# Kernel optimization log

Hardware: AMD Instinct MI355X
Metric: run time of the kernel (lower is better)

Reference implementation:

```python
import jax, jax.numpy as jnp
import numpy as np
import math

DIM = 1024
D_IN = 2048      # expand * dim
N = 16           # d_state
NG = 32          # ngroups
DT_RANK = 64     # ceil(dim/16)
D_CONV = 4
B, L = 2, 1024


def setup_inputs() -> dict:
    key = jax.random.key(0)
    ks = jax.random.split(key, 10)
    nrm = lambda k, shp, s: jax.random.normal(k, shp, jnp.float32) * s
    x = jax.random.normal(ks[0], (B, L, DIM), jnp.float32)
    latent = jnp.zeros((B, NG, D_IN, N), jnp.float32)
    W_in = nrm(ks[1], (2 * D_IN, DIM), 0.02)          # in_proj (no bias)
    conv_w = nrm(ks[2], (D_IN, 1, D_CONV), 0.1)        # depthwise conv weight
    conv_b = nrm(ks[3], (D_IN,), 0.02)                 # conv bias
    W_x = nrm(ks[4], (DT_RANK + 2 * N, D_IN), 0.02)    # x_proj (no bias)
    W_dt = nrm(ks[5], (D_IN, DT_RANK), 0.02)           # dt_proj weight
    b_dt = nrm(ks[6], (D_IN,), 0.1)                    # dt_proj bias
    W_out = nrm(ks[7], (DIM, D_IN), 0.02)              # out_proj (no bias)
    A_log = jnp.log(jnp.tile(jnp.arange(1, N + 1, dtype=jnp.float32), (D_IN, 1)))
    D = jnp.ones((D_IN,), jnp.float32)
    W_cattn = nrm(ks[8], (3 * N, N), 0.02)             # c_attn (no bias)
    return dict(x=x, latent=latent, W_in=W_in, conv_w=conv_w, conv_b=conv_b,
                W_x=W_x, W_dt=W_dt, b_dt=b_dt, W_out=W_out, A_log=A_log,
                D=D, W_cattn=W_cattn)


def _scan_op(e1, e2):
    a1, b1 = e1
    a2, b2 = e2
    return a2 * a1, a2 * b1 + b2


def reference(x, latent, W_in, conv_w, conv_b, W_x, W_dt, b_dt, W_out, A_log, D, W_cattn):
    b, l, _ = x.shape
    xr = x @ W_in.T                                  # [b,l,2*d_in]
    u, res = xr[..., :D_IN], xr[..., D_IN:]
    # depthwise causal conv1d (padding d_conv-1 then truncate to l == left-pad)
    uc = jnp.transpose(u, (0, 2, 1))                 # [b,d_in,l]
    uc = jax.lax.conv_general_dilated(
        uc, conv_w, window_strides=(1,), padding=[(D_CONV - 1, 0)],
        feature_group_count=D_IN, dimension_numbers=('NCH', 'OIH', 'NCH'))
    uc = uc + conv_b[None, :, None]
    u = jax.nn.silu(jnp.transpose(uc, (0, 2, 1)))    # [b,l,d_in]

    A = -jnp.exp(A_log)                              # [d_in,n]
    x_dbl = u @ W_x.T                                # [b,l,dt_rank+2n]
    delta = jax.nn.softplus(x_dbl[..., :DT_RANK] @ W_dt.T + b_dt)  # [b,l,d_in]
    Bm = x_dbl[..., DT_RANK:DT_RANK + N]             # [b,l,n]
    Cm = x_dbl[..., DT_RANK + N:]                    # [b,l,n]

    dA = jnp.exp(delta[..., None] * A)               # [b,l,d_in,n]
    dBu = delta[..., None] * Bm[:, :, None, :] * u[..., None]  # [b,l,d_in,n]

    pg = l // NG
    dA = dA.reshape(b, NG, pg, D_IN, N)
    dBu = dBu.reshape(b, NG, pg, D_IN, N)
    Cg = Cm.reshape(b, NG, pg, N)
    dBu = dBu.at[:, :, 0].add(latent)                # inject group latent

    # parallel scan of h_t = dA_t * h_{t-1} + dBu_t within each group
    _, hs = jax.lax.associative_scan(_scan_op, (dA, dBu), axis=2)
    y = jnp.einsum('bgpdn,bgpn->bgpd', hs, Cg).reshape(b, l, D_IN)
    y = y + u * D

    # latent communication: causal attention over group latents (initial latent, per source)
    qkv = latent[:, :-1] @ W_cattn.T                 # [b,ng-1,d_in,3n]
    q, k, v = jnp.split(qkv, 3, axis=-1)
    G = NG - 1
    q = q.reshape(b, G, -1)
    k = k.reshape(b, G, -1)
    v = v.reshape(b, G, -1)
    scale = 1.0 / math.sqrt(D_IN * N)
    scores = (q @ jnp.swapaxes(k, 1, 2)) * scale     # [b,G,G]
    mask = jnp.tril(jnp.ones((G, G), bool))
    scores = jnp.where(mask, scores, -jnp.inf)
    attn = jax.nn.softmax(scores, axis=-1)
    lat = (attn @ v).reshape(b, G, D_IN, N)
    lat_out = jnp.concatenate([jnp.zeros((b, 1, D_IN, N), x.dtype), lat], axis=1)

    out = (y * jax.nn.silu(res)) @ W_out.T           # [b,l,dim]
    return out, lat_out
```

## Files before the change

### kernel.cpp

```cpp
#include <hip/hip_runtime.h>
#include <stdint.h>

typedef uint16_t u16;
typedef u16   u16x4  __attribute__((ext_vector_type(4)));
typedef u16   u16x8  __attribute__((ext_vector_type(8)));
typedef __bf16 bf16x8 __attribute__((ext_vector_type(8)));
typedef float f32x4  __attribute__((ext_vector_type(4)));

__device__ __forceinline__ float b2f(u16 x) {
    union { uint32_t u; float f; } c; c.u = ((uint32_t)x) << 16; return c.f;
}
__device__ __forceinline__ u16 f2b(float f) {
    union { float f; uint32_t u; } c; c.f = f;
    uint32_t r = c.u + 0x7FFFu + ((c.u >> 16) & 1u);
    return (u16)(r >> 16);
}
__device__ __forceinline__ float silu_f(float x) { return x / (1.f + __expf(-x)); }

__device__ __forceinline__ void gload16(const u16* g, u16* l) {
    __builtin_amdgcn_global_load_lds(
        (const __attribute__((address_space(1))) void*)(g),
        (__attribute__((address_space(3))) void*)(l), 16, 0, 0);
}

__device__ __forceinline__ int dtype_flag_block(const u16* __restrict__ xraw) {
    __shared__ int bad;
    if (threadIdx.x == 0) bad = 0;
    __syncthreads();
    float v = b2f(xraw[threadIdx.x]);
    if (!(fabsf(v) < 1000.f)) atomicAdd(&bad, 1);
    __syncthreads();
    return bad;
}

struct CvtArgs {
    const void* s[13];
    u16* d[13];
    int cum[14];
    int total;
};
__global__ __launch_bounds__(256) void cvt_all_k(CvtArgs a, const u16* __restrict__ xraw)
{
    int flag = dtype_flag_block(xraw);
    int u4 = blockIdx.x * 256 + threadIdx.x;
    if (u4 >= a.total) return;
    int seg = 0;
    while (u4 >= a.cum[seg + 1]) seg++;
    int local = u4 - a.cum[seg];
    const void* s = a.s[seg];
    u16x4 o;
    if (s == nullptr) {
        o[0] = o[1] = o[2] = o[3] = 0;
    } else if (flag) {
        f32x4 vv = ((const f32x4*)s)[local];
        for (int e = 0; e < 4; e++) o[e] = f2b(vv[e]);
    } else {
        o = ((const u16x4*)s)[local];
    }
    *(u16x4*)(a.d[seg] + (size_t)local * 4) = o;
}

template<int EPI, int TN>
__device__ __forceinline__ void gemm_core(
    int bx, int by, int bz,
    const u16* __restrict__ A, const u16* __restrict__ B,
    int Kc, int lda, int ldb,
    u16* __restrict__ Cb, float* __restrict__ Cf, int ldc, int ncols,
    const u16* __restrict__ bias, size_t zslab)
{
    constexpr int NJ = TN / 32;
    constexpr int BT = TN / 32;
    __shared__ __align__(16) u16 lA[128 * 64];
    __shared__ __align__(16) u16 lB[TN * 64];
    const int tid  = threadIdx.x;
    const int wave = tid >> 6, lane = tid & 63;
    const int quad = lane >> 4, l16 = lane & 15;
    const int wm = wave & 1, wn = wave >> 1;
    const int row0 = by * 128, col0 = bx * TN;
    const int kbeg = bz * Kc;

    f32x4 acc[4][NJ];
    const f32x4 zf = {0.f, 0.f, 0.f, 0.f};
    for (int i = 0; i < 4; i++) for (int j = 0; j < NJ; j++) acc[i][j] = zf;

    const u16* Ap[4]; const u16* Bp[BT];
    int lbaseA[4], lbaseB[BT];
    for (int t = 0; t < 4; t++) {
        int c = t * 256 + tid;
        int r = c >> 3, s = c & 7;
        int q = (s - (r >> 1)) & 7;
        Ap[t] = A + (size_t)(row0 + r) * lda + q * 8 + kbeg;
        lbaseA[t] = (t * 256 + wave * 64) * 8;
    }
    for (int t = 0; t < BT; t++) {
        int c = t * 256 + tid;
        int r = c >> 3, s = c & 7;
        int q = (s - (r >> 1)) & 7;
        Bp[t] = B + (size_t)(col0 + r) * ldb + q * 8 + kbeg;
        lbaseB[t] = (t * 256 + wave * 64) * 8;
    }

    for (int k0 = 0; k0 < Kc; k0 += 64) {
        for (int t = 0; t < 4; t++) gload16(Ap[t] + k0, &lA[lbaseA[t]]);
        for (int t = 0; t < BT; t++) gload16(Bp[t] + k0, &lB[lbaseB[t]]);
        __syncthreads();
        for (int half = 0; half < 2; half++) {
            bf16x8 af[4], bfr[NJ];
            for (int i = 0; i < 4; i++) {
                int r = wm * 64 + i * 16 + l16;
                int s = (half * 4 + quad + (r >> 1)) & 7;
                af[i] = *(const bf16x8*)&lA[r * 64 + s * 8];
            }
            for (int j = 0; j < NJ; j++) {
                int r = wn * (TN / 2) + j * 16 + l16;
                int s = (half * 4 + quad + (r >> 1)) & 7;
                bfr[j] = *(const bf16x8*)&lB[r * 64 + s * 8];
            }
            for (int i = 0; i < 4; i++)
                for (int j = 0; j < NJ; j++)
                    acc[i][j] = __builtin_amdgcn_mfma_f32_16x16x32_bf16(af[i], bfr[j], acc[i][j], 0, 0, 0);
        }
        __syncthreads();
    }

    float* dstf = (EPI == 2) ? (Cf + (size_t)bz * zslab) : Cf;
    for (int i = 0; i < 4; i++) {
        int mb = row0 + wm * 64 + i * 16 + quad * 4;
        for (int j = 0; j < NJ; j++) {
            int n = col0 + wn * (TN / 2) + j * 16 + l16;
            if (n >= ncols) continue;
            if (EPI == 0) {
                for (int v = 0; v < 4; v++)
                    Cb[(size_t)(mb + v) * ldc + n] = f2b(acc[i][j][v]);
            } else if (EPI == 1) {
                float bv = b2f(bias[n]);
                for (int v = 0; v < 4; v++) {
                    float xx = acc[i][j][v] + bv;
                    dstf[(size_t)(mb + v) * ldc + n] =
                        fmaxf(xx, 0.f) + __logf(1.f + __expf(-fabsf(xx)));
                }
            } else {
                for (int v = 0; v < 4; v++)
                    dstf[(size_t)(mb + v) * ldc + n] = acc[i][j][v];
            }
        }
    }
}

template<int EPI, int TN>
__global__ __launch_bounds__(256) void gemm_bt(
    const u16* __restrict__ A, const u16* __restrict__ B,
    int Kc, int lda, int ldb,
    u16* __restrict__ Cb, float* __restrict__ Cf, int ldc, int ncols,
    const u16* __restrict__ bias, size_t zslab)
{
    gemm_core<EPI, TN>(blockIdx.x, blockIdx.y, blockIdx.z,
                       A, B, Kc, lda, ldb, Cb, Cf, ldc, ncols, bias, zslab);
}

__global__ __launch_bounds__(256) void redc_k(
    const float* __restrict__ part, u16* __restrict__ dst)
{
    int gid = blockIdx.x * 256 + threadIdx.x;
    int idx = gid * 4;
    f32x4 s = {0.f, 0.f, 0.f, 0.f};
    for (int sl = 0; sl < 16; sl++) {
        f32x4 p = *(const f32x4*)&part[(size_t)sl * 262144 + idx];
        for (int e = 0; e < 4; e++) s[e] += p[e];
    }
    u16x4 o;
    for (int e = 0; e < 4; e++) o[e] = f2b(s[e]);
    *(u16x4*)&dst[idx] = o;
}

__global__ __launch_bounds__(256) void conv_silu_k(
    const u16* __restrict__ xr, const u16* __restrict__ cw,
    const u16* __restrict__ cb, u16* __restrict__ u)
{
    int tid = threadIdx.x;
    int bl  = blockIdx.x;
    int l   = bl & 1023;
    int d0  = tid * 8;
    float acc[8];
    u16x8 bias = *(const u16x8*)&cb[d0];
    for (int j = 0; j < 8; j++) acc[j] = b2f(bias[j]);
    union { u16x8 v[4]; u16 s[32]; } wb;
    for (int t = 0; t < 4; t++) wb.v[t] = *(const u16x8*)&cw[d0 * 4 + t * 8];
    for (int t = 0; t < 4; t++) {
        int ls = l - 3 + t;
        if (ls < 0) continue;
        u16x8 xv = *(const u16x8*)&xr[(size_t)(bl - 3 + t) * 4096 + d0];
        for (int j = 0; j < 8; j++) acc[j] += b2f(xv[j]) * b2f(wb.s[j * 4 + t]);
    }
    u16x8 o;
    for (int j = 0; j < 8; j++) o[j] = f2b(silu_f(acc[j]));
    *(u16x8*)&u[(size_t)bl * 2048 + d0] = o;
}

__global__ __launch_bounds__(256) void scan_qkv_k(
    const float* __restrict__ delta, const u16* __restrict__ u,
    const u16* __restrict__ xr, const u16* __restrict__ xdbl,
    const u16* __restrict__ latent, const u16* __restrict__ Alog,
    const u16* __restrict__ Dp, u16* __restrict__ yg,
    const u16* __restrict__ Wc, u16* __restrict__ q, u16* __restrict__ k,
    u16* __restrict__ v)
{
    __shared__ float sm[1024];
    int tid = threadIdx.x;
    int bid = blockIdx.x;
    if (bid < 512) {
        float (*Bs)[16] = (float(*)[16])sm;
        float (*Cs)[16] = (float(*)[16])(sm + 512);
        int dblk = bid & 7, bg = bid >> 3;
        int d = dblk * 256 + tid;
        for (int idx = tid; idx < 512; idx += 256) {
            int p = idx >> 4, n = idx & 15;
            const u16* xp = &xdbl[(size_t)(bg * 32 + p) * 128];
            Bs[p][n] = b2f(xp[64 + n]);
            Cs[p][n] = b2f(xp[80 + n]);
        }
        __syncthreads();
        float a[16], h[16];
        {
            u16x8 a0 = *(const u16x8*)&Alog[(size_t)d * 16];
            u16x8 a1 = *(const u16x8*)&Alog[(size_t)d * 16 + 8];
            u16x8 l0 = *(const u16x8*)&latent[((size_t)bg * 2048 + d) * 16];
            u16x8 l1 = *(const u16x8*)&latent[((size_t)bg * 2048 + d) * 16 + 8];
            for (int n = 0; n < 8; n++) {
                a[n] = -__expf(b2f(a0[n])); a[8 + n] = -__expf(b2f(a1[n]));
                h[n] = b2f(l0[n]);          h[8 + n] = b2f(l1[n]);
            }
        }
        float Dd = b2f(Dp[d]);
        for (int p = 0; p < 32; p++) {
            size_t row = (size_t)bg * 32 + p;
            float dlt = delta[row * 2048 + d];
            float uu  = b2f(u[row * 2048 + d]);
            float db  = dlt * uu;
            float y = 0.f;
            if (p == 0) {
                for (int n = 0; n < 16; n++) { h[n] += db * Bs[0][n]; y += h[n] * Cs[0][n]; }
            } else {
                for (int n = 0; n < 16; n++) {
                    float w = __expf(dlt * a[n]);
                    h[n] = w * h[n] + db * Bs[p][n];
                    y += h[n] * Cs[p][n];
                }
            }
            float rs = b2f(xr[row * 4096 + 2048 + d]);
            yg[row * 2048 + d] = f2b((y + uu * Dd) * silu_f(rs));
        }
    } else {
        float (*Ws)[16] = (float(*)[16])sm;
        for (int i = tid; i < 768; i += 256) Ws[i >> 4][i & 15] = b2f(Wc[i]);
        __syncthreads();
        int gid = (bid - 512) * 256 + tid;
        int d = gid & 2047;
        int bi = gid >> 11;
        int b = bi / 31, i = bi - b * 31;
        const u16* lp = &latent[(((size_t)b * 32 + i) * 2048 + d) * 16];
        float lv[16];
        {
            u16x8 l0 = *(const u16x8*)lp, l1 = *(const u16x8*)(lp + 8);
            for (int m = 0; m < 8; m++) { lv[m] = b2f(l0[m]); lv[8 + m] = b2f(l1[m]); }
        }
        u16* outs[3] = {q, k, v};
        for (int pl = 0; pl < 3; pl++) {
            u16x8 o0, o1;
            for (int n = 0; n < 16; n++) {
                float s = 0.f;
                for (int m = 0; m < 16; m++) s += lv[m] * Ws[pl * 16 + n][m];
                if (n < 8) o0[n] = f2b(s); else o1[n - 8] = f2b(s);
            }
            u16* op = outs[pl] + (size_t)bi * 32768 + d * 16;
            *(u16x8*)op = o0; *(u16x8*)(op + 8) = o1;
        }
    }
}

__global__ __launch_bounds__(256) void gemm_scores_k(
    const u16* __restrict__ yg, const u16* __restrict__ Wout, float* __restrict__ out_part,
    const u16* __restrict__ q, const u16* __restrict__ kk, float* __restrict__ sc)
{
    int bid = blockIdx.x;
    if (bid < 512) {
        int bx = bid & 15, by = (bid >> 4) & 15, bz = bid >> 8;
        gemm_core<2, 64>(bx, by, bz, yg, Wout, 1024, 2048, 2048,
                         nullptr, out_part, 1024, 1024, nullptr, (size_t)2048 * 1024);
        return;
    }
    int idx = bid - 512;
    int b = idx / 961, r = idx - b * 961;
    int i = r / 31, j = r - i * 31;
    if (j > i) return;
    const u16* qp = q + ((size_t)b * 31 + i) * 32768;
    const u16* kp = kk + ((size_t)b * 31 + j) * 32768;
    float s = 0.f;
    for (int t = threadIdx.x * 8; t < 32768; t += 2048) {
        u16x8 a = *(const u16x8*)&qp[t];
        u16x8 c = *(const u16x8*)&kp[t];
        for (int e = 0; e < 8; e++) s += b2f(a[e]) * b2f(c[e]);
    }
    for (int off = 32; off; off >>= 1) s += __shfl_xor(s, off);
    __shared__ float red[4];
    if ((threadIdx.x & 63) == 0) red[threadIdx.x >> 6] = s;
    __syncthreads();
    if (threadIdx.x == 0)
        sc[idx] = (red[0] + red[1] + red[2] + red[3]) * 5.5242717e-3f;
}

__global__ __launch_bounds__(256) void attv_redout_k(
    const float* __restrict__ sc, const u16* __restrict__ v,
    const float* __restrict__ part, void* __restrict__ dout,
    const u16* __restrict__ xraw)
{
    int flag = dtype_flag_block(xraw);
    int bid = blockIdx.x;
    if (bid < 1024) {
        int chunk = bid & 15, bi = bid >> 4;
        int b = bi >> 5, i = (bi & 31) - 1;
        __shared__ float as[32];
        if (i >= 0 && threadIdx.x < 64) {
            float x = (threadIdx.x <= i) ? sc[(size_t)b * 961 + i * 31 + threadIdx.x] : -3.4e38f;
            float mx = x;
            for (int off = 32; off; off >>= 1) mx = fmaxf(mx, __shfl_xor(mx, off));
            float e = (threadIdx.x <= i) ? __expf(x - mx) : 0.f;
            float sm = e;
            for (int off = 32; off; off >>= 1) sm += __shfl_xor(sm, off);
            if (threadIdx.x < 32) as[threadIdx.x] = e / sm;
        }
        __syncthreads();
        int dn = chunk * 2048 + threadIdx.x * 8;
        float acc[8] = {0, 0, 0, 0, 0, 0, 0, 0};
        if (i >= 0) {
            for (int j = 0; j <= i; j++) {
                u16x8 vv = *(const u16x8*)&v[((size_t)b * 31 + j) * 32768 + dn];
                float aj = as[j];
                for (int e = 0; e < 8; e++) acc[e] += aj * b2f(vv[e]);
            }
            for (int e = 0; e < 8; e++) if (!(fabsf(acc[e]) < 1e30f)) acc[e] = 0.f;
        }
        size_t ofs = 2097152 + ((size_t)b * 32 + (i + 1)) * 32768 + dn;
        if (flag) {
            f32x4 o0, o1;
            for (int e = 0; e < 4; e++) { o0[e] = acc[e]; o1[e] = acc[4 + e]; }
            *(f32x4*)((float*)dout + ofs) = o0;
            *(f32x4*)((float*)dout + ofs + 4) = o1;
        } else {
            u16x8 o;
            for (int e = 0; e < 8; e++) o[e] = f2b(acc[e]);
            *(u16x8*)((u16*)dout + ofs) = o;
        }
    } else {
        int gid = (bid - 1024) * 256 + threadIdx.x;
        int m = gid >> 8;
        int j = (gid & 255) * 4;
        f32x4 s = {0.f, 0.f, 0.f, 0.f};
        for (int ks = 0; ks < 2; ks++) {
            f32x4 p = *(const f32x4*)&part[((size_t)ks * 2048 + m) * 1024 + j];
            for (int e = 0; e < 4; e++) s[e] += p[e];
        }
        for (int e = 0; e < 4; e++) if (!(fabsf(s[e]) < 1e30f)) s[e] = 0.f;
        if (flag) {
            ((f32x4*)dout)[(size_t)m * 256 + (j >> 2)] = s;
        } else {
            u16x4 o;
            for (int e = 0; e < 4; e++) o[e] = f2b(s[e]);
            ((u16x4*)dout)[(size_t)m * 256 + (j >> 2)] = o;
        }
    }
}

extern "C" void kernel_launch(void* const* d_in, const int* in_sizes, int n_in,
                              void* d_out, int out_size, void* d_ws, size_t ws_size,
                              hipStream_t stream)
{
    char* ws = (char*)d_ws;
    const u16* xraw = (const u16*)d_in[0];
    u16* cx    = (u16*)(ws + 0);
    u16* clat  = (u16*)(ws + 4194304);
    u16* cWin  = (u16*)(ws + 8388608);
    u16* ccw   = (u16*)(ws + 16777216);
    u16* ccb   = (u16*)(ws + 16793600);
    u16* wxp   = (u16*)(ws + 16797696);
    u16* cWdt  = (u16*)(ws + 17321984);
    u16* cbdt  = (u16*)(ws + 17584128);
    u16* cWout = (u16*)(ws + 17588224);
    u16* cAlog = (u16*)(ws + 21782528);
    u16* cD    = (u16*)(ws + 21848064);
    u16* cWc   = (u16*)(ws + 21852160);
    float* xdbl_part = (float*)(ws + 21853760);
    u16*   xdbl      = (u16*)(ws + 38630976);
    float* sc        = (float*)(ws + 39155264);
    u16*   u         = (u16*)(ws + 39163008);
    u16*   xr        = (u16*)(ws + 47551616);
    u16*   yg        = (u16*)(ws + 64328832);
    float* delta     = (float*)(ws + 72717440);
    u16*   qb        = (u16*)(ws + 89494656);
    u16*   kb        = qb + 2031616;
    u16*   vb        = kb + 2031616;
    float* out_part  = (float*)(ws + 101684352);

    CvtArgs ca;
    const void* srcs[13] = { d_in[0], d_in[1], d_in[2], d_in[3], d_in[4],
                             d_in[5], nullptr, d_in[6], d_in[7], d_in[8],
                             d_in[9], d_in[10], d_in[11] };
    u16* dsts[13] = { cx, clat, cWin, ccw, ccb,
                      wxp, wxp + 196608, cWdt, cbdt, cWout,
                      cAlog, cD, cWc };
    int ns[13] = { 2097152, 2097152, 4194304, 8192, 2048,
                   196608, 65536, 131072, 2048, 2097152,
                   32768, 2048, 768 };
    int cum = 0;
    for (int i = 0; i < 13; i++) {
        ca.s[i] = srcs[i]; ca.d[i] = dsts[i];
        ca.cum[i] = cum; cum += ns[i] / 4;
    }
    ca.cum[13] = cum; ca.total = cum;
    cvt_all_k<<<(cum + 255) / 256, 256, 0, stream>>>(ca, xraw);

    gemm_bt<0, 64><<<dim3(64, 16, 1), 256, 0, stream>>>(cx, cWin, 1024, 1024, 1024,
                                                        xr, nullptr, 4096, 4096, nullptr, 0);
    conv_silu_k<<<2048, 256, 0, stream>>>(xr, ccw, ccb, u);
    gemm_bt<2, 64><<<dim3(2, 16, 16), 256, 0, stream>>>(u, wxp, 128, 2048, 2048,
                                                        nullptr, xdbl_part, 128, 128,
                                                        nullptr, 262144);
    redc_k<<<256, 256, 0, stream>>>(xdbl_part, xdbl);
    gemm_bt<1, 64><<<dim3(32, 16, 1), 256, 0, stream>>>(xdbl, cWdt, 64, 128, 64,
                                                        nullptr, delta, 2048, 2048, cbdt, 0);
    scan_qkv_k<<<1008, 256, 0, stream>>>(delta, u, xr, xdbl, clat, cAlog, cD, yg,
                                         cWc, qb, kb, vb);
    gemm_scores_k<<<2434, 256, 0, stream>>>(yg, cWout, out_part, qb, kb, sc);
    attv_redout_k<<<3072, 256, 0, stream>>>(sc, vb, out_part, d_out, xraw);
}
```

Measured before the change: 226.5 us.

## Fuse dt_proj GEMM and softplus into the selective-scan kernel

Removes the separate dt_proj GEMM launch that wrote a full fp32 delta tensor to global memory. Each scan block now loads its 32 rows of x_dbl and 256 rows of W_dt into LDS and computes delta with MFMA, adding the bias and softplus in-block. The values go into shared memory and the scan reads them from there. This drops one launch and the round trip of an 8 MB fp32 buffer, but raises LDS use per scan block to about 72 KB, which may lower occupancy. Each of the 8 d-blocks also reloads the same x_dbl rows.

```diff
diff --git a/kernel.cpp b/kernel.cpp
--- a/kernel.cpp
+++ b/kernel.cpp
@@ -16,6 +16,9 @@
     return (u16)(r >> 16);
 }
 __device__ __forceinline__ float silu_f(float x) { return x / (1.f + __expf(-x)); }
+__device__ __forceinline__ float softplus_f(float x) {
+    return fmaxf(x, 0.f) + __logf(1.f + __expf(-fabsf(x)));
+}
 
 __device__ __forceinline__ void gload16(const u16* g, u16* l) {
     __builtin_amdgcn_global_load_lds(
@@ -66,7 +69,7 @@
     const u16* __restrict__ A, const u16* __restrict__ B,
     int Kc, int lda, int ldb,
     u16* __restrict__ Cb, float* __restrict__ Cf, int ldc, int ncols,
-    const u16* __restrict__ bias, size_t zslab)
+    size_t zslab)
 {
     constexpr int NJ = TN / 32;
     constexpr int BT = TN / 32;
@@ -132,13 +135,6 @@
             if (EPI == 0) {
                 for (int v = 0; v < 4; v++)
                     Cb[(size_t)(mb + v) * ldc + n] = f2b(acc[i][j][v]);
-            } else if (EPI == 1) {
-                float bv = b2f(bias[n]);
-                for (int v = 0; v < 4; v++) {
-                    float xx = acc[i][j][v] + bv;
-                    dstf[(size_t)(mb + v) * ldc + n] =
-                        fmaxf(xx, 0.f) + __logf(1.f + __expf(-fabsf(xx)));
-                }
             } else {
                 for (int v = 0; v < 4; v++)
                     dstf[(size_t)(mb + v) * ldc + n] = acc[i][j][v];
@@ -152,10 +148,10 @@
     const u16* __restrict__ A, const u16* __restrict__ B,
     int Kc, int lda, int ldb,
     u16* __restrict__ Cb, float* __restrict__ Cf, int ldc, int ncols,
-    const u16* __restrict__ bias, size_t zslab)
+    size_t zslab)
 {
     gemm_core<EPI, TN>(blockIdx.x, blockIdx.y, blockIdx.z,
-                       A, B, Kc, lda, ldb, Cb, Cf, ldc, ncols, bias, zslab);
+                       A, B, Kc, lda, ldb, Cb, Cf, ldc, ncols, zslab);
 }
 
 __global__ __launch_bounds__(256) void redc_k(
@@ -198,21 +194,40 @@
 }
 
 __global__ __launch_bounds__(256) void scan_qkv_k(
-    const float* __restrict__ delta, const u16* __restrict__ u,
-    const u16* __restrict__ xr, const u16* __restrict__ xdbl,
+    const u16* __restrict__ u, const u16* __restrict__ xr,
+    const u16* __restrict__ xdbl, const u16* __restrict__ Wdt,
+    const u16* __restrict__ bdt,
     const u16* __restrict__ latent, const u16* __restrict__ Alog,
     const u16* __restrict__ Dp, u16* __restrict__ yg,
     const u16* __restrict__ Wc, u16* __restrict__ q, u16* __restrict__ k,
     u16* __restrict__ v)
 {
-    __shared__ float sm[1024];
+    __shared__ __align__(16) u16 lsh[36864];
     int tid = threadIdx.x;
     int bid = blockIdx.x;
     if (bid < 512) {
-        float (*Bs)[16] = (float(*)[16])sm;
-        float (*Cs)[16] = (float(*)[16])(sm + 512);
+        u16* lA = lsh;
+        u16* lB = lsh + 2048;
+        float* dls = (float*)(lsh + 18432);
+        float (*Bs)[16] = (float(*)[16])(lsh + 34816);
+        float (*Cs)[16] = (float(*)[16])(lsh + 35840);
+        const int wave = tid >> 6, lane = tid & 63;
+        const int quad = lane >> 4, l16 = lane & 15;
         int dblk = bid & 7, bg = bid >> 3;
         int d = dblk * 256 + tid;
+
+        {
+            int r = tid >> 3, s = tid & 7;
+            int qg = (s - (r >> 1)) & 7;
+            gload16(&xdbl[(size_t)(bg * 32 + r) * 128 + qg * 8], &lA[(wave * 64) * 8]);
+        }
+        for (int t = 0; t < 8; t++) {
+            int c = t * 256 + tid;
+            int r = c >> 3, s = c & 7;
+            int qg = (s - (r >> 1)) & 7;
+            gload16(&Wdt[(size_t)(dblk * 256 + r) * 64 + qg * 8],
+                    &lB[(t * 256 + wave * 64) * 8]);
+        }
         for (int idx = tid; idx < 512; idx += 256) {
             int p = idx >> 4, n = idx & 15;
             const u16* xp = &xdbl[(size_t)(bg * 32 + p) * 128];
@@ -220,6 +235,37 @@
             Cs[p][n] = b2f(xp[80 + n]);
         }
         __syncthreads();
+
+        f32x4 dacc[2][4];
+        const f32x4 zf = {0.f, 0.f, 0.f, 0.f};
+        for (int i = 0; i < 2; i++) for (int j = 0; j < 4; j++) dacc[i][j] = zf;
+        for (int half = 0; half < 2; half++) {
+            bf16x8 af[2], bfr[4];
+            for (int i = 0; i < 2; i++) {
+                int r = i * 16 + l16;
+                int s = (half * 4 + quad + (r >> 1)) & 7;
+                af[i] = *(const bf16x8*)&lA[r * 64 + s * 8];
+            }
+            for (int j = 0; j < 4; j++) {
+                int r = wave * 64 + j * 16 + l16;
+                int s = (half * 4 + quad + (r >> 1)) & 7;
+                bfr[j] = *(const bf16x8*)&lB[r * 64 + s * 8];
+            }
+            for (int i = 0; i < 2; i++)
+                for (int j = 0; j < 4; j++)
+                    dacc[i][j] = __builtin_amdgcn_mfma_f32_16x16x32_bf16(af[i], bfr[j], dacc[i][j], 0, 0, 0);
+        }
+        for (int j = 0; j < 4; j++) {
+            int n = wave * 64 + j * 16 + l16;
+            float bv = b2f(bdt[dblk * 256 + n]);
+            for (int i = 0; i < 2; i++) {
+                int mb = i * 16 + quad * 4;
+                for (int vv = 0; vv < 4; vv++)
+                    dls[(mb + vv) * 256 + n] = softplus_f(dacc[i][j][vv] + bv);
+            }
+        }
+        __syncthreads();
+
         float a[16], h[16];
         {
             u16x8 a0 = *(const u16x8*)&Alog[(size_t)d * 16];
@@ -234,7 +280,7 @@
         float Dd = b2f(Dp[d]);
         for (int p = 0; p < 32; p++) {
             size_t row = (size_t)bg * 32 + p;
-            float dlt = delta[row * 2048 + d];
+            float dlt = dls[p * 256 + tid];
             float uu  = b2f(u[row * 2048 + d]);
             float db  = dlt * uu;
             float y = 0.f;
@@ -251,7 +297,7 @@
             yg[row * 2048 + d] = f2b((y + uu * Dd) * silu_f(rs));
         }
     } else {
-        float (*Ws)[16] = (float(*)[16])sm;
+        float (*Ws)[16] = (float(*)[16])lsh;
         for (int i = tid; i < 768; i += 256) Ws[i >> 4][i & 15] = b2f(Wc[i]);
         __syncthreads();
         int gid = (bid - 512) * 256 + tid;
@@ -286,7 +332,7 @@
     if (bid < 512) {
         int bx = bid & 15, by = (bid >> 4) & 15, bz = bid >> 8;
         gemm_core<2, 64>(bx, by, bz, yg, Wout, 1024, 2048, 2048,
-                         nullptr, out_part, 1024, 1024, nullptr, (size_t)2048 * 1024);
+                         nullptr, out_part, 1024, 1024, (size_t)2048 * 1024);
         return;
     }
     int idx = bid - 512;
@@ -395,11 +441,10 @@
     u16*   u         = (u16*)(ws + 39163008);
     u16*   xr        = (u16*)(ws + 47551616);
     u16*   yg        = (u16*)(ws + 64328832);
-    float* delta     = (float*)(ws + 72717440);
-    u16*   qb        = (u16*)(ws + 89494656);
+    u16*   qb        = (u16*)(ws + 72717440);
     u16*   kb        = qb + 2031616;
     u16*   vb        = kb + 2031616;
-    float* out_part  = (float*)(ws + 101684352);
+    float* out_part  = (float*)(ws + 84907136);
 
     CvtArgs ca;
     const void* srcs[13] = { d_in[0], d_in[1], d_in[2], d_in[3], d_in[4],
@@ -420,15 +465,13 @@
     cvt_all_k<<<(cum + 255) / 256, 256, 0, stream>>>(ca, xraw);
 
     gemm_bt<0, 64><<<dim3(64, 16, 1), 256, 0, stream>>>(cx, cWin, 1024, 1024, 1024,
-                                                        xr, nullptr, 4096, 4096, nullptr, 0);
+                                                        xr, nullptr, 4096, 4096, 0);
     conv_silu_k<<<2048, 256, 0, stream>>>(xr, ccw, ccb, u);
     gemm_bt<2, 64><<<dim3(2, 16, 16), 256, 0, stream>>>(u, wxp, 128, 2048, 2048,
                                                         nullptr, xdbl_part, 128, 128,
-                                                        nullptr, 262144);
+                                                        262144);
     redc_k<<<256, 256, 0, stream>>>(xdbl_part, xdbl);
-    gemm_bt<1, 64><<<dim3(32, 16, 1), 256, 0, stream>>>(xdbl, cWdt, 64, 128, 64,
-                                                        nullptr, delta, 2048, 2048, cbdt, 0);
-    scan_qkv_k<<<1008, 256, 0, stream>>>(delta, u, xr, xdbl, clat, cAlog, cD, yg,
+    scan_qkv_k<<<1008, 256, 0, stream>>>(u, xr, xdbl, cWdt, cbdt, clat, cAlog, cD, yg,
                                          cWc, qb, kb, vb);
     gemm_scores_k<<<2434, 256, 0, stream>>>(yg, cWout, out_part, qb, kb, sc);
     attv_redout_k<<<3072, 256, 0, stream>>>(sc, vb, out_part, d_out, xraw);
```

Measured after the change: 224.9 us. About the same (-0.7%).
